# Performance work log

Measured on AMD Instinct MI355X. Metric: run time of the kernel, lower is better.

## Reference

```python
import jax, jax.numpy as jnp
import numpy as np
from jax import lax

TOPN = 4
CAT_NUM = 4
NUM_CLS = 200
PAD = 224
IMG = 448
HP = IMG + 2 * PAD  # 896
CROP = 224
IOU_THRESH = 0.25


def _gen_edge_anchors():
    # generate_default_anchor_maps: 3 pyramid levels; anchors ordered (anchor, h, w)
    # per level to match the channel-first flatten of ProposalNet tidy outputs.
    settings = [
        (32, 48.0, [2 ** (1. / 3.), 2 ** (2. / 3.)], [0.667, 1.0, 1.5]),
        (64, 96.0, [2 ** (1. / 3.), 2 ** (2. / 3.)], [0.667, 1.0, 1.5]),
        (128, 192.0, [1.0, 2 ** (1. / 3.), 2 ** (2. / 3.)], [0.667, 1.0, 1.5]),
    ]
    blocks = []
    for stride, size, scales, ars in settings:
        n = int(np.ceil(IMG / stride))
        c = np.arange(n, dtype=np.float64) * stride + stride / 2.0
        cy, cx = np.meshgrid(c, c, indexing='ij')
        for sc in scales:
            for ar in ars:
                h = size * sc / np.sqrt(ar)
                w = size * sc * np.sqrt(ar)
                a = np.stack([cy - h / 2., cx - w / 2., cy + h / 2., cx + w / 2.], axis=-1)
                blocks.append(a.reshape(-1, 4))
    e = np.concatenate(blocks, axis=0)  # [1614, 4] (y0,x0,y1,x1)
    return (e + PAD).astype(np.int32)   # offset into padded image, truncated to int


EDGE_ANCHORS = _gen_edge_anchors()


def _conv(x, w, b, stride, pad):
    y = lax.conv_general_dilated(x, w, (stride, stride), [(pad, pad), (pad, pad)],
                                 dimension_numbers=('NCHW', 'OIHW', 'NCHW'))
    return y + b[None, :, None, None]


def _proposal_net(x, d1w, d1b, d2w, d2b, d3w, d3b, t1w, t1b, t2w, t2b, t3w, t3b):
    B = x.shape[0]
    d1 = jax.nn.relu(_conv(x, d1w, d1b, 1, 1))   # [B,128,14,14]
    d2 = jax.nn.relu(_conv(d1, d2w, d2b, 2, 1))  # [B,128,7,7]
    d3 = jax.nn.relu(_conv(d2, d3w, d3b, 2, 1))  # [B,128,4,4]
    t1 = _conv(d1, t1w, t1b, 1, 0).reshape(B, -1)  # 6*14*14 = 1176
    t2 = _conv(d2, t2w, t2b, 1, 0).reshape(B, -1)  # 6*7*7  = 294
    t3 = _conv(d3, t3w, t3b, 1, 0).reshape(B, -1)  # 9*4*4  = 144
    return jnp.concatenate([t1, t2, t3], axis=1)   # [B,1614]


def _hard_nms(scores, boxes, area):
    # Greedy hard NMS over A anchors, returns TOPN kept indices (score-desc order).
    A = scores.shape[0]

    def body(k, carry):
        mask, idxs = carry
        i = jnp.argmax(jnp.where(mask, scores, -jnp.inf))
        b = boxes[i]
        yy0 = jnp.maximum(boxes[:, 0], b[0])
        xx0 = jnp.maximum(boxes[:, 1], b[1])
        yy1 = jnp.minimum(boxes[:, 2], b[2])
        xx1 = jnp.minimum(boxes[:, 3], b[3])
        inter = jnp.maximum(yy1 - yy0, 0.) * jnp.maximum(xx1 - xx0, 0.)
        iou = inter / (area + area[i] - inter)
        mask = (mask & (iou < IOU_THRESH)).at[i].set(False)
        return mask, idxs.at[k].set(i.astype(jnp.int32))

    _, idxs = lax.fori_loop(0, TOPN, body, (jnp.ones((A,), bool), jnp.zeros((TOPN,), jnp.int32)))
    return idxs


def _crop_resize(img, box):
    # img [3,HP,HP], box [4] float (integer-valued). Bilinear, align_corners=True:
    # src coord = y0 + i*(h-1)/(CROP-1) over the slice [y0:y1).
    y0, x0, y1, x1 = box[0], box[1], box[2], box[3]
    t = jnp.arange(CROP, dtype=jnp.float32) / (CROP - 1.)
    ys = y0 + t * (y1 - y0 - 1.)
    xs = x0 + t * (x1 - x0 - 1.)
    yi0 = jnp.clip(jnp.floor(ys).astype(jnp.int32), 0, HP - 1)
    xi0 = jnp.clip(jnp.floor(xs).astype(jnp.int32), 0, HP - 1)
    yi1 = jnp.minimum(yi0 + 1, HP - 1)
    xi1 = jnp.minimum(xi0 + 1, HP - 1)
    wy = (ys - yi0.astype(jnp.float32))[None, :, None]
    wx = (xs - xi0.astype(jnp.float32))[None, None, :]
    r0 = img[:, yi0, :]
    r1 = img[:, yi1, :]
    rows = r0 + (r1 - r0) * wy          # [3,CROP,HP]
    c0 = rows[:, :, xi0]
    c1 = rows[:, :, xi1]
    return c0 + (c1 - c0) * wx          # [3,CROP,CROP]


def reference(x, rpn_feature, feature, resnet_out,
              down1_w, down1_b, down2_w, down2_b, down3_w, down3_b,
              tidy1_w, tidy1_b, tidy2_w, tidy2_b, tidy3_w, tidy3_b,
              feat_w, feat_b, partcls_w, partcls_b, concat_w, concat_b):
    B = x.shape[0]
    boxes_f = jnp.asarray(EDGE_ANCHORS, jnp.float32)
    area = (boxes_f[:, 2] - boxes_f[:, 0]) * (boxes_f[:, 3] - boxes_f[:, 1])

    rpn_score = _proposal_net(lax.stop_gradient(rpn_feature),
                              down1_w, down1_b, down2_w, down2_b, down3_w, down3_b,
                              tidy1_w, tidy1_b, tidy2_w, tidy2_b, tidy3_w, tidy3_b)
    scores_sg = lax.stop_gradient(rpn_score)
    top_idx = jax.vmap(lambda s: _hard_nms(s, boxes_f, area))(scores_sg)   # [B,TOPN]
    top_n_prob = jnp.take_along_axis(rpn_score, top_idx, axis=1)           # [B,TOPN]

    x_pad = jnp.pad(x, ((0, 0), (0, 0), (PAD, PAD), (PAD, PAD)))           # [B,3,896,896]
    sel_boxes = boxes_f[top_idx]                                           # [B,TOPN,4]
    part_imgs = jax.vmap(lambda img, bxs: jax.vmap(lambda b: _crop_resize(img, b))(bxs))(x_pad, sel_boxes)
    part_imgs = lax.stop_gradient(part_imgs).reshape(B * TOPN, 3, CROP, CROP)  # detach()

    # per-crop feature trunk (stand-in for shared ResNet50): strided 7x7 conv + GAP
    pf = jax.nn.relu(_conv(part_imgs, feat_w, feat_b, 32, 3)).mean(axis=(2, 3))  # [B*TOPN,2048]
    part_logits = (pf @ partcls_w.T + partcls_b).reshape(B, TOPN, NUM_CLS)
    part_feature = pf.reshape(B, TOPN, -1)[:, :CAT_NUM].reshape(B, -1)           # [B,4*2048]
    concat_out = jnp.concatenate([part_feature, feature], axis=1)                # [B,10240]
    concat_logits = concat_out @ concat_w.T + concat_b
    return resnet_out, concat_logits, part_logits, top_idx, top_n_prob


def setup_inputs():
    key = jax.random.key(0)
    ks = jax.random.split(key, 13)
    B = 16
    n = lambda k, shp, s=1.0: jax.random.normal(k, shp, jnp.float32) * s
    z = lambda c: jnp.zeros((c,), jnp.float32)
    return {
        'x': n(ks[0], (B, 3, 448, 448)),
        'rpn_feature': jax.nn.relu(n(ks[1], (B, 2048, 14, 14))),
        'feature': n(ks[2], (B, 2048)),
        'resnet_out': n(ks[3], (B, 200)),
        'down1_w': n(ks[4], (128, 2048, 3, 3), 0.01),
        'down1_b': z(128),
        'down2_w': n(ks[5], (128, 128, 3, 3), 0.03),
        'down2_b': z(128),
        'down3_w': n(ks[6], (128, 128, 3, 3), 0.03),
        'down3_b': z(128),
        'tidy1_w': n(ks[7], (6, 128, 1, 1), 0.1),
        'tidy1_b': z(6),
        'tidy2_w': n(ks[8], (6, 128, 1, 1), 0.1),
        'tidy2_b': z(6),
        'tidy3_w': n(ks[9], (9, 128, 1, 1), 0.1),
        'tidy3_b': z(9),
        'feat_w': n(ks[10], (2048, 3, 7, 7), 0.05),
        'feat_b': z(2048),
        'partcls_w': n(ks[11], (200, 2048), 0.02),
        'partcls_b': z(200),
        'concat_w': n(ks[12], (200, 2048 * (CAT_NUM + 1)), 0.01),
        'concat_b': z(200),
    }
```

## Files before the change

### kernel.cpp

```cpp
#include <hip/hip_runtime.h>
#include <math.h>

#define NANCH 1614
#define A1 1176
#define A2 1470
#define KSPLIT 4
#define N_D1E (16*128*196)

#define OFF_D1 0
#define OFF_D2 401408
#define OFF_D3 501760
#define OFF_SC 534528
#define OFF_PF 560352
#define OFF_P  691424
#define OFF_INT 1152416
#define OFF_BIG 1158944
#define SZ_AT 3211264
#define SZ_BW 1179648
#define OFF_ATH (OFF_BIG)
#define OFF_ATL (OFF_ATH + SZ_AT)
#define OFF_BWH (OFF_ATL + SZ_AT)
#define OFF_BWL (OFF_BWH + SZ_BW)
#define OFF_PM  (OFF_BWL + SZ_BW)
#define SZ_PM   3612672
#define TOTAL_MFMA_F (OFF_PM + SZ_PM)
#define N_D2E (16*128*49)
#define N_D3E (16*128*16)
#define OFF_P2 OFF_BIG
#define OFF_P3 (OFF_BIG + 4*N_D2E)

#define OUT_CONCAT 3200
#define OUT_PART   6400
#define OUT_TIDX   19200
#define OUT_TPROB  19264

typedef __attribute__((ext_vector_type(8))) short short8;
typedef __attribute__((ext_vector_type(4))) float f32x4;

__device__ __forceinline__ unsigned short bf16_rn(float f) {
    unsigned u = __float_as_uint(f);
    unsigned r = u + 0x7fffu + ((u >> 16) & 1u);
    return (unsigned short)(r >> 16);
}
__device__ __forceinline__ float bf16_to_f(unsigned short h) {
    return __uint_as_float(((unsigned)h) << 16);
}

__global__ void anchor_kernel(int* __restrict__ anc) {
    int i = blockIdx.x * 256 + threadIdx.x;
    if (i >= NANCH) return;
    int stride, n, sgroup, j;
    double size;
    if (i < A1)      { stride = 32;  size = 48.0;  n = 14; j = i;      sgroup = 0; }
    else if (i < A2) { stride = 64;  size = 96.0;  n = 7;  j = i - A1; sgroup = 0; }
    else             { stride = 128; size = 192.0; n = 4;  j = i - A2; sgroup = 1; }
    int cells = n * n;
    int combo = j / cells, cell = j % cells;
    int sc_i = combo / 3, ar_i = combo % 3;
    double sc;
    if (sgroup == 0) sc = pow(2.0, (double)(sc_i + 1) / 3.0);
    else             sc = (sc_i == 0) ? 1.0 : pow(2.0, (double)sc_i / 3.0);
    double ar = (ar_i == 0) ? 0.667 : ((ar_i == 1) ? 1.0 : 1.5);
    int y = cell / n, x = cell % n;
    double cy = (double)y * stride + stride / 2.0;
    double cx = (double)x * stride + stride / 2.0;
    double sq = sqrt(ar);
    double h = size * sc / sq, w = size * sc * sq;
    anc[i*4+0] = (int)(cy - h/2.0 + 224.0);
    anc[i*4+1] = (int)(cx - w/2.0 + 224.0);
    anc[i*4+2] = (int)(cy + h/2.0 + 224.0);
    anc[i*4+3] = (int)(cx + w/2.0 + 224.0);
}

__launch_bounds__(256)
__global__ void split_rpn_t(const float* __restrict__ rpn,
                            unsigned short* __restrict__ ath, unsigned short* __restrict__ atl) {
    __shared__ float T[32*197];
    int b = blockIdx.x >> 6, icb = blockIdx.x & 63;
    int tid = threadIdx.x;
    for (int idx = tid; idx < 32*196; idx += 256) {
        int i = idx / 196, s = idx % 196;
        T[i*197 + s] = rpn[((size_t)(b*2048 + icb*32 + i))*196 + s];
    }
    __syncthreads();
    for (int idx = tid; idx < 32*196; idx += 256) {
        int s = idx >> 5, i = idx & 31;
        float f = T[i*197 + s];
        unsigned short hi = bf16_rn(f);
        unsigned short lo = bf16_rn(f - bf16_to_f(hi));
        size_t o = ((size_t)(b*196 + s))*2048 + icb*32 + i;
        ath[o] = hi; atl[o] = lo;
    }
}

__global__ void split_w(const float* __restrict__ w1,
                        unsigned short* __restrict__ bwh, unsigned short* __restrict__ bwl) {
    int idx = blockIdx.x * 256 + threadIdx.x;
    if (idx >= 9*128*2048) return;
    int tap = idx / (128*2048);
    int rem = idx % (128*2048);
    int oc = rem >> 11, ic = rem & 2047;
    float f = w1[((size_t)(oc*2048 + ic))*9 + tap];
    unsigned short hi = bf16_rn(f);
    unsigned short lo = bf16_rn(f - bf16_to_f(hi));
    bwh[idx] = hi; bwl[idx] = lo;
}

__launch_bounds__(256)
__global__ void d1_mfma(const unsigned short* __restrict__ ath, const unsigned short* __restrict__ atl,
                        const unsigned short* __restrict__ bwh, const unsigned short* __restrict__ bwl,
                        float* __restrict__ partM) {
    __shared__ unsigned short Ah[32*40], Al[32*40], Bh[128*40], Bl[128*40];
    int tid = threadIdx.x;
    int mb = blockIdx.x % 98, tap = blockIdx.x / 98;
    int dy = tap/3 - 1, dx = tap%3 - 1;
    int wave = tid >> 6, lane = tid & 63;
    int wr = wave >> 1, wc = wave & 1;
    int lg = lane >> 4, lr = lane & 15;

    int ar = tid >> 3, ahalf = (tid >> 2) & 1, aslot = tid & 3;
    int grow = mb*32 + ar;
    int b = grow / 196, s = grow % 196;
    int y = s / 14, x = s % 14;
    int ys = y + dy, xs = x + dx;
    bool avalid = (ys >= 0) && (ys < 14) && (xs >= 0) && (xs < 14);
    const unsigned short* asrc = (ahalf ? atl : ath)
        + ((size_t)(b*196 + (avalid ? (ys*14 + xs) : 0)))*2048 + aslot*8;
    unsigned short* adst = (ahalf ? Al : Ah) + ar*40 + aslot*8;

    const unsigned short* bsrc[4]; unsigned short* bdst[4];
#pragma unroll
    for (int rep = 0; rep < 4; ++rep) {
        int idx = rep*256 + tid;
        int half = idx >> 9, u = idx & 511, oc = u >> 2, slot = u & 3;
        bsrc[rep] = (half ? bwl : bwh) + ((size_t)(tap*128 + oc))*2048 + slot*8;
        bdst[rep] = (half ? Bl : Bh) + oc*40 + slot*8;
    }

    f32x4 acc[4];
#pragma unroll
    for (int f = 0; f < 4; ++f) acc[f] = (f32x4){0.f, 0.f, 0.f, 0.f};
    const short8 zer = {0,0,0,0,0,0,0,0};

    short8 ga, gb[4];
    ga = avalid ? *(const short8*)(asrc) : zer;
#pragma unroll
    for (int rep = 0; rep < 4; ++rep) gb[rep] = *(const short8*)(bsrc[rep]);

    for (int step = 0; step < 64; ++step) {
        __syncthreads();
        *(short8*)adst = ga;
#pragma unroll
        for (int rep = 0; rep < 4; ++rep) *(short8*)bdst[rep] = gb[rep];
        __syncthreads();
        if (step + 1 < 64) {
            int ic0 = (step + 1) * 32;
            ga = avalid ? *(const short8*)(asrc + ic0) : zer;
#pragma unroll
            for (int rep = 0; rep < 4; ++rep) gb[rep] = *(const short8*)(bsrc[rep] + ic0);
        }
        short8 a_h = *(const short8*)&Ah[(wr*16 + lr)*40 + lg*8];
        short8 a_l = *(const short8*)&Al[(wr*16 + lr)*40 + lg*8];
#pragma unroll
        for (int f = 0; f < 4; ++f) {
            int oc = wc*64 + f*16 + lr;
            short8 b_h = *(const short8*)&Bh[oc*40 + lg*8];
            short8 b_l = *(const short8*)&Bl[oc*40 + lg*8];
            acc[f] = __builtin_amdgcn_mfma_f32_16x16x32_bf16(a_h, b_h, acc[f], 0, 0, 0);
            acc[f] = __builtin_amdgcn_mfma_f32_16x16x32_bf16(a_h, b_l, acc[f], 0, 0, 0);
            acc[f] = __builtin_amdgcn_mfma_f32_16x16x32_bf16(a_l, b_h, acc[f], 0, 0, 0);
        }
    }
#pragma unroll
    for (int f = 0; f < 4; ++f) {
        int oc = wc*64 + f*16 + lr;
#pragma unroll
        for (int r = 0; r < 4; ++r) {
            int row = mb*32 + wr*16 + lg*4 + r;
            partM[((size_t)tap*3136 + row)*128 + oc] = acc[f][r];
        }
    }
}

__global__ void d1_combine(const float* __restrict__ partM, const float* __restrict__ b1,
                           float* __restrict__ d1) {
    int idx = blockIdx.x*256 + threadIdx.x;
    if (idx >= 3136*128) return;
    int oc = idx & 127, row = idx >> 7;
    float s = 0.f;
#pragma unroll
    for (int t = 0; t < 9; ++t) s += partM[(size_t)t*3136*128 + idx];
    int b = row / 196, sp = row % 196;
    d1[(b*128 + oc)*196 + sp] = fmaxf(s + b1[oc], 0.f);
}

__launch_bounds__(256)
__global__ void conv_d1_part(const float* __restrict__ rpn, const float* __restrict__ w1,
                             float* __restrict__ part) {
    __shared__ float lin[8*256];
    __shared__ float lwT[576];
    int tid = threadIdx.x;
    int ks = blockIdx.x & 3;
    int tile = (blockIdx.x >> 2) & 15;
    int b = blockIdx.x >> 6;
    int py = tid >> 4, px = tid & 15;
    bool pvalid = (py >= 1) && (py <= 14) && (px >= 1) && (px <= 14);
    int in_off = (b*2048)*196 + (py-1)*14 + (px-1);
    const float* wb = w1 + tile*8*18432;
    int s = tid, y = s / 14, x = s % 14;
    bool active = s < 196;
    float acc[8];
#pragma unroll
    for (int o = 0; o < 8; ++o) acc[o] = 0.f;
    float pv[8]; float wv[3];
    int c0 = ks * 64;
#pragma unroll
    for (int i = 0; i < 8; ++i) pv[i] = pvalid ? rpn[in_off + (c0*8 + i)*196] : 0.f;
#pragma unroll
    for (int r = 0; r < 3; ++r) {
        int u = tid + r*256;
        if (u < 576) { int oc = u/72, rem = u%72; wv[r] = wb[oc*18432 + c0*72 + rem]; }
    }
    for (int c = 0; c < 64; ++c) {
#pragma unroll
        for (int i = 0; i < 8; ++i) lin[i*256 + tid] = pv[i];
#pragma unroll
        for (int r = 0; r < 3; ++r) {
            int u = tid + r*256;
            if (u < 576) { int oc = u/72, rem = u%72; lwT[rem*8 + oc] = wv[r]; }
        }
        __syncthreads();
        if (c + 1 < 64) {
            int icb = (c0 + c + 1) * 8;
#pragma unroll
            for (int i = 0; i < 8; ++i) pv[i] = pvalid ? rpn[in_off + (icb + i)*196] : 0.f;
#pragma unroll
            for (int r = 0; r < 3; ++r) {
                int u = tid + r*256;
                if (u < 576) { int oc = u/72, rem = u%72; wv[r] = wb[oc*18432 + icb*9 + rem]; }
            }
        }
        if (active) {
#pragma unroll
            for (int ic = 0; ic < 8; ++ic) {
                int base = ic*256 + y*16 + x;
                float p[9];
                p[0]=lin[base+0];  p[1]=lin[base+1];  p[2]=lin[base+2];
                p[3]=lin[base+16]; p[4]=lin[base+17]; p[5]=lin[base+18];
                p[6]=lin[base+32]; p[7]=lin[base+33]; p[8]=lin[base+34];
#pragma unroll
                for (int k = 0; k < 9; ++k) {
                    const float4 wa  = *(const float4*)&lwT[(ic*9 + k)*8];
                    const float4 wb4 = *(const float4*)&lwT[(ic*9 + k)*8 + 4];
                    acc[0] += p[k]*wa.x;  acc[1] += p[k]*wa.y;
                    acc[2] += p[k]*wa.z;  acc[3] += p[k]*wa.w;
                    acc[4] += p[k]*wb4.x; acc[5] += p[k]*wb4.y;
                    acc[6] += p[k]*wb4.z; acc[7] += p[k]*wb4.w;
                }
            }
        }
        __syncthreads();
    }
    if (active) {
#pragma unroll
        for (int o = 0; o < 8; ++o) {
            int oc = tile*8 + o;
            part[ks*N_D1E + (b*128 + oc)*196 + s] = acc[o];
        }
    }
}

__global__ void d1_reduce(const float* __restrict__ part, const float* __restrict__ b1,
                          float* __restrict__ d1) {
    int idx = blockIdx.x * 256 + threadIdx.x;
    if (idx >= N_D1E) return;
    int oc = (idx / 196) & 127;
    float s = part[idx] + part[idx + N_D1E] + part[idx + 2*N_D1E] + part[idx + 3*N_D1E];
    d1[idx] = fmaxf(s + b1[oc], 0.f);
}

__launch_bounds__(256)
__global__ void conv_d2_part(const float* __restrict__ d1, const float* __restrict__ w2,
                             float* __restrict__ part) {
    __shared__ float lin[8*320];
    __shared__ float lwT[72*32];
    int tid = threadIdx.x;
    int ks = blockIdx.x & 3;
    int octile = (blockIdx.x >> 2) & 3;
    int b = blockIdx.x >> 4;
    int py = tid >> 4, px = tid & 15;
    bool pvalid = (py >= 1) && (py <= 14) && (px >= 1) && (px <= 14);
    int in_base = (b*128)*196 + (py-1)*14 + (px-1);
    int g = tid >> 6, s = tid & 63;
    int yo = s / 7, xo = s % 7;
    bool active = s < 49;
    const float* wb = w2 + (octile*32)*1152 + ks*288;

    float acc[8];
#pragma unroll
    for (int o = 0; o < 8; ++o) acc[o] = 0.f;
    float pv[8], wv[9];
#pragma unroll
    for (int i = 0; i < 8; ++i) pv[i] = pvalid ? d1[in_base + (ks*32 + i)*196] : 0.f;
#pragma unroll
    for (int r = 0; r < 9; ++r) {
        int u = tid + r*256; int oc_l = u/72, rem = u%72;
        wv[r] = wb[oc_l*1152 + rem];
    }
    for (int c = 0; c < 4; ++c) {
#pragma unroll
        for (int i = 0; i < 8; ++i) lin[i*320 + py*20 + px] = pv[i];
#pragma unroll
        for (int r = 0; r < 9; ++r) {
            int u = tid + r*256; int oc_l = u/72, rem = u%72;
            lwT[rem*32 + oc_l] = wv[r];
        }
        __syncthreads();
        if (c + 1 < 4) {
            int ic0 = ks*32 + (c+1)*8;
#pragma unroll
            for (int i = 0; i < 8; ++i) pv[i] = pvalid ? d1[in_base + (ic0 + i)*196] : 0.f;
#pragma unroll
            for (int r = 0; r < 9; ++r) {
                int u = tid + r*256; int oc_l = u/72, rem = u%72;
                wv[r] = wb[oc_l*1152 + (c+1)*72 + rem];
            }
        }
        if (active) {
#pragma unroll
            for (int ic = 0; ic < 8; ++ic) {
                int base = ic*320 + (2*yo)*20 + 2*xo;
                float p[9];
                p[0]=lin[base+0];  p[1]=lin[base+1];  p[2]=lin[base+2];
                p[3]=lin[base+20]; p[4]=lin[base+21]; p[5]=lin[base+22];
                p[6]=lin[base+40]; p[7]=lin[base+41]; p[8]=lin[base+42];
#pragma unroll
                for (int k = 0; k < 9; ++k) {
                    const float4 wa  = *(const float4*)&lwT[(ic*9 + k)*32 + g*8];
                    const float4 wb4 = *(const float4*)&lwT[(ic*9 + k)*32 + g*8 + 4];
                    acc[0] += p[k]*wa.x;  acc[1] += p[k]*wa.y;
                    acc[2] += p[k]*wa.z;  acc[3] += p[k]*wa.w;
                    acc[4] += p[k]*wb4.x; acc[5] += p[k]*wb4.y;
                    acc[6] += p[k]*wb4.z; acc[7] += p[k]*wb4.w;
                }
            }
        }
        __syncthreads();
    }
    if (active) {
#pragma unroll
        for (int o = 0; o < 8; ++o) {
            int oc = octile*32 + g*8 + o;
            part[ks*N_D2E + (b*128 + oc)*49 + s] = acc[o];
        }
    }
}

__launch_bounds__(256)
__global__ void conv_d3_part(const float* __restrict__ d2, const float* __restrict__ w3,
                             float* __restrict__ part) {
    __shared__ float lin3[8*108];
    __shared__ float lwT3[72*128];
    int tid = threadIdx.x;
    int ks = blockIdx.x & 15;
    int b = blockIdx.x >> 4;
    int g = tid >> 4, s = tid & 15;
    int yo = s >> 2, xo = s & 3;

    for (int r = 0; r < 4; ++r) {
        int u = tid + r*256;
        if (u < 864) {
            int ic = u / 108, rem = u % 108;
            int ty = rem / 12, tx = rem % 12;
            int iy = ty - 1, ix = tx - 1;
            float v = 0.f;
            if (iy >= 0 && iy < 7 && ix >= 0 && ix < 7)
                v = d2[(b*128 + ks*8 + ic)*49 + iy*7 + ix];
            lin3[u] = v;
        }
    }
#pragma unroll
    for (int r = 0; r < 36; ++r) {
        int u = tid + r*256;
        int oc_l = u / 72, rem = u % 72;
        lwT3[rem*128 + oc_l] = w3[oc_l*1152 + ks*72 + rem];
    }
    __syncthreads();

    float acc[8];
#pragma unroll
    for (int o = 0; o < 8; ++o) acc[o] = 0.f;
#pragma unroll
    for (int ic = 0; ic < 8; ++ic) {
        int base = ic*108 + (2*yo)*12 + 2*xo;
        float p[9];
        p[0]=lin3[base+0];  p[1]=lin3[base+1];  p[2]=lin3[base+2];
        p[3]=lin3[base+12]; p[4]=lin3[base+13]; p[5]=lin3[base+14];
        p[6]=lin3[base+24]; p[7]=lin3[base+25]; p[8]=lin3[base+26];
#pragma unroll
        for (int k = 0; k < 9; ++k) {
            const float4 wa  = *(const float4*)&lwT3[(ic*9 + k)*128 + g*8];
            const float4 wb4 = *(const float4*)&lwT3[(ic*9 + k)*128 + g*8 + 4];
            acc[0] += p[k]*wa.x;  acc[1] += p[k]*wa.y;
            acc[2] += p[k]*wa.z;  acc[3] += p[k]*wa.w;
            acc[4] += p[k]*wb4.x; acc[5] += p[k]*wb4.y;
            acc[6] += p[k]*wb4.z; acc[7] += p[k]*wb4.w;
        }
    }
#pragma unroll
    for (int o = 0; o < 8; ++o) {
        int oc = g*8 + o;
        part[ks*N_D3E + (b*128 + oc)*16 + s] = acc[o];
    }
}

__global__ void reduce_relu(const float* __restrict__ part, const float* __restrict__ bias,
                            float* __restrict__ out, int nsplit, int N, int SP) {
    int idx = blockIdx.x*256 + threadIdx.x;
    if (idx >= N) return;
    int oc = (idx / SP) & 127;
    float s = 0.f;
    for (int p = 0; p < nsplit; ++p) s += part[p*N + idx];
    out[idx] = fmaxf(s + bias[oc], 0.f);
}

__global__ void tidy_kernel(const float* __restrict__ d1, const float* __restrict__ d2, const float* __restrict__ d3,
                            const float* __restrict__ t1w, const float* __restrict__ t1b,
                            const float* __restrict__ t2w, const float* __restrict__ t2b,
                            const float* __restrict__ t3w, const float* __restrict__ t3b,
                            float* __restrict__ scores) {
    int idx = blockIdx.x * 256 + threadIdx.x;
    if (idx >= 16*NANCH) return;
    int b = idx / NANCH, i = idx % NANCH;
    const float* src; const float* tw; const float* tb; int S, c, s;
    if (i < A1)      { c = i/196;           s = i%196;        src = d1 + b*128*196 + s; S = 196; tw = t1w; tb = t1b; }
    else if (i < A2) { int j = i - A1; c = j/49; s = j%49;    src = d2 + b*128*49  + s; S = 49;  tw = t2w; tb = t2b; }
    else             { int j = i - A2; c = j/16; s = j%16;    src = d3 + b*128*16  + s; S = 16;  tw = t3w; tb = t3b; }
    float acc = tb[c];
    const float* wr = tw + c*128;
    for (int ic = 0; ic < 128; ++ic) acc += src[ic*S] * wr[ic];
    scores[idx] = acc;
}

__launch_bounds__(256)
__global__ void nms_kernel(const float* __restrict__ scores, const int* __restrict__ anc,
                           int* __restrict__ topidx, float* __restrict__ out) {
    __shared__ float s[NANCH];
    __shared__ float by0[NANCH], bx0[NANCH], by1[NANCH], bx1[NANCH], ar[NANCH];
    __shared__ float rv[256]; __shared__ int ri[256];
    __shared__ int sel[4];
    int b = blockIdx.x, tid = threadIdx.x;
    for (int j = tid; j < NANCH; j += 256) {
        s[j] = scores[b*NANCH + j];
        float y0 = (float)anc[j*4+0], x0 = (float)anc[j*4+1];
        float y1 = (float)anc[j*4+2], x1 = (float)anc[j*4+3];
        by0[j] = y0; bx0[j] = x0; by1[j] = y1; bx1[j] = x1;
        ar[j] = (y1 - y0) * (x1 - x0);
    }
    __syncthreads();
    for (int k = 0; k < 4; ++k) {
        float bv = -INFINITY; int bi = NANCH;
        for (int j = tid; j < NANCH; j += 256) {
            float v = s[j];
            if (v > bv) { bv = v; bi = j; }
        }
        rv[tid] = bv; ri[tid] = bi;
        __syncthreads();
        for (int off = 128; off > 0; off >>= 1) {
            if (tid < off) {
                float v2 = rv[tid+off]; int i2 = ri[tid+off];
                if (v2 > rv[tid] || (v2 == rv[tid] && i2 < ri[tid])) { rv[tid] = v2; ri[tid] = i2; }
            }
            __syncthreads();
        }
        int i = ri[0];
        if (tid == 0) sel[k] = i;
        float a0 = by0[i], a1 = bx0[i], a2 = by1[i], a3 = bx1[i], ai = ar[i];
        for (int j = tid; j < NANCH; j += 256) {
            float yy0 = fmaxf(by0[j], a0), xx0 = fmaxf(bx0[j], a1);
            float yy1 = fminf(by1[j], a2), xx1 = fminf(bx1[j], a3);
            float inter = fmaxf(yy1 - yy0, 0.f) * fmaxf(xx1 - xx0, 0.f);
            float iou = inter / (ar[j] + ai - inter);
            if (!(iou < 0.25f)) s[j] = -INFINITY;
        }
        if (tid == 0) s[i] = -INFINITY;
        __syncthreads();
    }
    if (tid < 4) {
        int i = sel[tid];
        topidx[b*4 + tid] = i;
        out[OUT_TIDX  + b*4 + tid] = (float)i;
        out[OUT_TPROB + b*4 + tid] = scores[b*NANCH + i];
    }
}

__device__ __forceinline__ float fetchpix(const float* img, int Y, int X) {
    if (Y >= 224 && Y < 672 && X >= 224 && X < 672) return img[(Y - 224)*448 + (X - 224)];
    return 0.f;
}

__global__ void sampler_kernel(const float* __restrict__ x, const int* __restrict__ anc,
                               const int* __restrict__ topidx, float* __restrict__ P) {
    int crop = blockIdx.x >> 2;
    int b = crop >> 2;
    int idx = topidx[crop];
    float y0 = (float)anc[idx*4+0], x0 = (float)anc[idx*4+1];
    float y1 = (float)anc[idx*4+2], x1 = (float)anc[idx*4+3];
    float dy = y1 - y0 - 1.0f, dx = x1 - x0 - 1.0f;
    const float* imgb = x + b*3*448*448;
    for (int u = (blockIdx.x & 3)*256 + threadIdx.x; u < 7203; u += 1024) {
        int c = u / 2401; int rem = u % 2401;
        int rid = rem / 49, cid = rem % 49;
        int oy = rid/7, ky = rid%7, ox = cid/7, kx = cid%7;
        int rr = 32*oy - 3 + ky, cc = 32*ox - 3 + kx;
        float val = 0.f;
        if (rr >= 0 && cc >= 0) {
            float ty = (float)rr / 223.0f;
            float ys = __fadd_rn(y0, __fmul_rn(ty, dy));
            int yi0 = (int)floorf(ys); yi0 = yi0 < 0 ? 0 : (yi0 > 895 ? 895 : yi0);
            int yi1 = (yi0 + 1 > 895) ? 895 : yi0 + 1;
            float wy = ys - (float)yi0;
            float tx = (float)cc / 223.0f;
            float xs = __fadd_rn(x0, __fmul_rn(tx, dx));
            int xi0 = (int)floorf(xs); xi0 = xi0 < 0 ? 0 : (xi0 > 895 ? 895 : xi0);
            int xi1 = (xi0 + 1 > 895) ? 895 : xi0 + 1;
            float wx = xs - (float)xi0;
            const float* img = imgb + c*448*448;
            float p00 = fetchpix(img, yi0, xi0), p10 = fetchpix(img, yi1, xi0);
            float p01 = fetchpix(img, yi0, xi1), p11 = fetchpix(img, yi1, xi1);
            float r0 = p00 + (p10 - p00)*wy;
            float r1 = p01 + (p11 - p01)*wy;
            val = r0 + (r1 - r0)*wx;
        }
        int pos = oy*7 + ox, kk = c*49 + ky*7 + kx;
        P[crop*7203 + pos*147 + kk] = val;
    }
}

__launch_bounds__(256)
__global__ void feat_gemm_kernel(const float* __restrict__ P, const float* __restrict__ fw,
                                 const float* __restrict__ fb, float* __restrict__ pf) {
    __shared__ float lp[49*148];
    int crop = blockIdx.x >> 3, tile = blockIdx.x & 7;
    int oc = tile*256 + threadIdx.x;
    for (int u = threadIdx.x; u < 7203; u += 256)
        lp[(u/147)*148 + (u%147)] = P[crop*7203 + u];
    __syncthreads();
    float s[49];
#pragma unroll
    for (int p = 0; p < 49; ++p) s[p] = 0.f;
    const float* wr = fw + oc*147;
    for (int kc = 0; kc < 36; ++kc) {
        float w0 = wr[kc*4], w1 = wr[kc*4+1], w2 = wr[kc*4+2], w3 = wr[kc*4+3];
#pragma unroll
        for (int p = 0; p < 49; ++p) {
            float4 v = *(const float4*)&lp[p*148 + kc*4];
            s[p] += v.x*w0 + v.y*w1 + v.z*w2 + v.w*w3;
        }
    }
    {
        float w0 = wr[144], w1 = wr[145], w2 = wr[146];
#pragma unroll
        for (int p = 0; p < 49; ++p)
            s[p] += lp[p*148+144]*w0 + lp[p*148+145]*w1 + lp[p*148+146]*w2;
    }
    float bias = fb[oc], acc = 0.f;
#pragma unroll
    for (int p = 0; p < 49; ++p) acc += fmaxf(s[p] + bias, 0.f);
    pf[crop*2048 + oc] = acc / 49.0f;
}

__global__ void partcls_kernel(const float* __restrict__ pf, const float* __restrict__ pw,
                               const float* __restrict__ pb, float* __restrict__ out) {
    int o = blockIdx.x; int crop = o / 200, cls = o % 200;
    int lane = threadIdx.x;
    const float* a = pf + crop*2048; const float* w = pw + cls*2048;
    float sum = 0.f;
#pragma unroll
    for (int i = 0; i < 8; ++i) {
        int k = lane*4 + i*256;
        float4 a4 = *(const float4*)&a[k];
        float4 w4 = *(const float4*)&w[k];
        sum += a4.x*w4.x + a4.y*w4.y + a4.z*w4.z + a4.w*w4.w;
    }
#pragma unroll
    for (int off = 32; off > 0; off >>= 1) sum += __shfl_down(sum, off);
    if (lane == 0) out[OUT_PART + o] = sum + pb[cls];
}

__launch_bounds__(256)
__global__ void concat_kernel(const float* __restrict__ pf, const float* __restrict__ feature,
                              const float* __restrict__ cw, const float* __restrict__ cb,
                              float* __restrict__ out) {
    __shared__ float red[4][16];
    int j = blockIdx.x, tid = threadIdx.x;
    const float* w = cw + (size_t)j*10240;
    float acc[16];
#pragma unroll
    for (int b = 0; b < 16; ++b) acc[b] = 0.f;
    for (int k = tid; k < 10240; k += 256) {
        float wk = w[k];
        const float* v; int stride;
        if (k < 8192) { v = pf + k; stride = 8192; }
        else          { v = feature + (k - 8192); stride = 2048; }
#pragma unroll
        for (int b = 0; b < 16; ++b) acc[b] += v[b*stride] * wk;
    }
#pragma unroll
    for (int b = 0; b < 16; ++b) {
        float s2 = acc[b];
#pragma unroll
        for (int off = 32; off > 0; off >>= 1) s2 += __shfl_down(s2, off);
        if ((tid & 63) == 0) red[tid >> 6][b] = s2;
    }
    __syncthreads();
    if (tid < 16)
        out[OUT_CONCAT + tid*200 + j] = red[0][tid] + red[1][tid] + red[2][tid] + red[3][tid] + cb[j];
}

extern "C" void kernel_launch(void* const* d_in, const int* in_sizes, int n_in,
                              void* d_out, int out_size, void* d_ws, size_t ws_size,
                              hipStream_t stream) {
    const float* x    = (const float*)d_in[0];
    const float* rpn  = (const float*)d_in[1];
    const float* feat = (const float*)d_in[2];
    const float* rout = (const float*)d_in[3];
    const float* d1w  = (const float*)d_in[4];
    const float* d1b  = (const float*)d_in[5];
    const float* d2w  = (const float*)d_in[6];
    const float* d2b  = (const float*)d_in[7];
    const float* d3w  = (const float*)d_in[8];
    const float* d3b  = (const float*)d_in[9];
    const float* t1w  = (const float*)d_in[10];
    const float* t1b  = (const float*)d_in[11];
    const float* t2w  = (const float*)d_in[12];
    const float* t2b  = (const float*)d_in[13];
    const float* t3w  = (const float*)d_in[14];
    const float* t3b  = (const float*)d_in[15];
    const float* fw   = (const float*)d_in[16];
    const float* fbb  = (const float*)d_in[17];
    const float* pw   = (const float*)d_in[18];
    const float* pb   = (const float*)d_in[19];
    const float* cw   = (const float*)d_in[20];
    const float* cb   = (const float*)d_in[21];
    float* out = (float*)d_out;
    float* wsf = (float*)d_ws;
    float* d1  = wsf + OFF_D1;
    float* d2  = wsf + OFF_D2;
    float* d3  = wsf + OFF_D3;
    float* sc  = wsf + OFF_SC;
    float* pfb = wsf + OFF_PF;
    float* P   = wsf + OFF_P;
    int* anc    = (int*)(wsf + OFF_INT);
    int* topidx = anc + NANCH*4;

    hipMemcpyAsync(out, rout, 3200*sizeof(float), hipMemcpyDeviceToDevice, stream);

    anchor_kernel<<<7, 256, 0, stream>>>(anc);

    bool use_mfma = ws_size >= (size_t)TOTAL_MFMA_F * sizeof(float);
    if (use_mfma) {
        unsigned short* ath = (unsigned short*)(wsf + OFF_ATH);
        unsigned short* atl = (unsigned short*)(wsf + OFF_ATL);
        unsigned short* bwh = (unsigned short*)(wsf + OFF_BWH);
        unsigned short* bwl = (unsigned short*)(wsf + OFF_BWL);
        float* pm = wsf + OFF_PM;
        split_rpn_t<<<1024, 256, 0, stream>>>(rpn, ath, atl);
        split_w<<<9216, 256, 0, stream>>>(d1w, bwh, bwl);
        d1_mfma<<<98*9, 256, 0, stream>>>(ath, atl, bwh, bwl, pm);
        d1_combine<<<(3136*128 + 255)/256, 256, 0, stream>>>(pm, d1b, d1);
    } else {
        float* part = wsf + OFF_BIG;
        conv_d1_part<<<16*16*KSPLIT, 256, 0, stream>>>(rpn, d1w, part);
        d1_reduce<<<(N_D1E + 255)/256, 256, 0, stream>>>(part, d1b, d1);
    }

    float* part2 = wsf + OFF_P2;
    float* part3 = wsf + OFF_P3;
    conv_d2_part<<<256, 256, 0, stream>>>(d1, d2w, part2);
    reduce_relu<<<(N_D2E + 255)/256, 256, 0, stream>>>(part2, d2b, d2, 4, N_D2E, 49);
    conv_d3_part<<<256, 256, 0, stream>>>(d2, d3w, part3);
    reduce_relu<<<(N_D3E + 255)/256, 256, 0, stream>>>(part3, d3b, d3, 16, N_D3E, 16);

    tidy_kernel<<<101, 256, 0, stream>>>(d1, d2, d3, t1w, t1b, t2w, t2b, t3w, t3b, sc);
    nms_kernel<<<16, 256, 0, stream>>>(sc, anc, topidx, out);
    sampler_kernel<<<256, 256, 0, stream>>>(x, anc, topidx, P);
    feat_gemm_kernel<<<512, 256, 0, stream>>>(P, fw, fbb, pfb);
    partcls_kernel<<<12800, 64, 0, stream>>>(pfb, pw, pb, out);
    concat_kernel<<<200, 256, 0, stream>>>(pfb, feat, cw, cb, out);
}
```

Baseline: 412.4 us.

## Double-buffer LDS and widen M tile to 64 rows in d1 MFMA conv

The d1 MFMA kernel now gives each block 64 output rows instead of 32, so every wave computes two 16-row fragments that share the same B-weight fragments. This halves how often the weight tile is reloaded per output and halves the grid to 441 blocks. Shared memory is double-buffered so the next K-step's global loads are written to the alternate buffer while MFMAs run, needing one barrier per step instead of two. The cost is more LDS and accumulator registers, which may lower occupancy, and fewer blocks for the CUs to share.

```diff
diff --git a/kernel.cpp b/kernel.cpp
--- a/kernel.cpp
+++ b/kernel.cpp
@@ -106,78 +106,109 @@
     bwh[idx] = hi; bwl[idx] = lo;
 }
 
+#define ABUF (64*40)
+#define BBUF (128*40)
 __launch_bounds__(256)
 __global__ void d1_mfma(const unsigned short* __restrict__ ath, const unsigned short* __restrict__ atl,
                         const unsigned short* __restrict__ bwh, const unsigned short* __restrict__ bwl,
                         float* __restrict__ partM) {
-    __shared__ unsigned short Ah[32*40], Al[32*40], Bh[128*40], Bl[128*40];
+    __shared__ unsigned short Ah[2*ABUF], Al[2*ABUF], Bh[2*BBUF], Bl[2*BBUF];
     int tid = threadIdx.x;
-    int mb = blockIdx.x % 98, tap = blockIdx.x / 98;
+    int tap = blockIdx.x / 49, mb = blockIdx.x % 49;
     int dy = tap/3 - 1, dx = tap%3 - 1;
     int wave = tid >> 6, lane = tid & 63;
     int wr = wave >> 1, wc = wave & 1;
     int lg = lane >> 4, lr = lane & 15;
 
-    int ar = tid >> 3, ahalf = (tid >> 2) & 1, aslot = tid & 3;
-    int grow = mb*32 + ar;
-    int b = grow / 196, s = grow % 196;
-    int y = s / 14, x = s % 14;
-    int ys = y + dy, xs = x + dx;
-    bool avalid = (ys >= 0) && (ys < 14) && (xs >= 0) && (xs < 14);
-    const unsigned short* asrc = (ahalf ? atl : ath)
-        + ((size_t)(b*196 + (avalid ? (ys*14 + xs) : 0)))*2048 + aslot*8;
-    unsigned short* adst = (ahalf ? Al : Ah) + ar*40 + aslot*8;
-
+    const unsigned short* asrc[2]; unsigned short* adst[2]; bool avalid[2];
+#pragma unroll
+    for (int rep = 0; rep < 2; ++rep) {
+        int idx = rep*256 + tid;
+        int rw = idx >> 3, half = (idx >> 2) & 1, slot = idx & 3;
+        int grow = mb*64 + rw;
+        int b = grow / 196, s = grow % 196;
+        int y = s / 14, x = s % 14;
+        int ys = y + dy, xs = x + dx;
+        bool av = (ys >= 0) && (ys < 14) && (xs >= 0) && (xs < 14);
+        avalid[rep] = av;
+        asrc[rep] = (half ? atl : ath)
+            + ((size_t)(b*196 + (av ? (ys*14 + xs) : 0)))*2048 + slot*8;
+        adst[rep] = (half ? Al : Ah) + rw*40 + slot*8;
+    }
     const unsigned short* bsrc[4]; unsigned short* bdst[4];
 #pragma unroll
     for (int rep = 0; rep < 4; ++rep) {
         int idx = rep*256 + tid;
-        int half = idx >> 9, u = idx & 511, oc = u >> 2, slot = u & 3;
+        int oc = idx >> 3, half = (idx >> 2) & 1, slot = idx & 3;
         bsrc[rep] = (half ? bwl : bwh) + ((size_t)(tap*128 + oc))*2048 + slot*8;
         bdst[rep] = (half ? Bl : Bh) + oc*40 + slot*8;
     }
 
-    f32x4 acc[4];
-#pragma unroll
-    for (int f = 0; f < 4; ++f) acc[f] = (f32x4){0.f, 0.f, 0.f, 0.f};
+    f32x4 acc[2][4];
+#pragma unroll
+    for (int r2 = 0; r2 < 2; ++r2)
+#pragma unroll
+        for (int f = 0; f < 4; ++f) acc[r2][f] = (f32x4){0.f, 0.f, 0.f, 0.f};
     const short8 zer = {0,0,0,0,0,0,0,0};
 
-    short8 ga, gb[4];
-    ga = avalid ? *(const short8*)(asrc) : zer;
+    short8 ga[2], gb[4];
+#pragma unroll
+    for (int rep = 0; rep < 2; ++rep) ga[rep] = avalid[rep] ? *(const short8*)(asrc[rep]) : zer;
 #pragma unroll
     for (int rep = 0; rep < 4; ++rep) gb[rep] = *(const short8*)(bsrc[rep]);
+#pragma unroll
+    for (int rep = 0; rep < 2; ++rep) *(short8*)(adst[rep]) = ga[rep];
+#pragma unroll
+    for (int rep = 0; rep < 4; ++rep) *(short8*)(bdst[rep]) = gb[rep];
+    __syncthreads();
+
+    int abase_w = wr*32*40 + lr*40 + lg*8;
+    int bbase_w = wc*64*40 + lg*8;
 
     for (int step = 0; step < 64; ++step) {
-        __syncthreads();
-        *(short8*)adst = ga;
-#pragma unroll
-        for (int rep = 0; rep < 4; ++rep) *(short8*)bdst[rep] = gb[rep];
-        __syncthreads();
+        int buf = step & 1;
         if (step + 1 < 64) {
             int ic0 = (step + 1) * 32;
-            ga = avalid ? *(const short8*)(asrc + ic0) : zer;
+#pragma unroll
+            for (int rep = 0; rep < 2; ++rep) ga[rep] = avalid[rep] ? *(const short8*)(asrc[rep] + ic0) : zer;
 #pragma unroll
             for (int rep = 0; rep < 4; ++rep) gb[rep] = *(const short8*)(bsrc[rep] + ic0);
         }
-        short8 a_h = *(const short8*)&Ah[(wr*16 + lr)*40 + lg*8];
-        short8 a_l = *(const short8*)&Al[(wr*16 + lr)*40 + lg*8];
+        int ab = buf*ABUF, bb = buf*BBUF;
+        short8 ah0 = *(const short8*)&Ah[ab + abase_w];
+        short8 ah1 = *(const short8*)&Ah[ab + abase_w + 16*40];
+        short8 al0 = *(const short8*)&Al[ab + abase_w];
+        short8 al1 = *(const short8*)&Al[ab + abase_w + 16*40];
 #pragma unroll
         for (int f = 0; f < 4; ++f) {
-            int oc = wc*64 + f*16 + lr;
-            short8 b_h = *(const short8*)&Bh[oc*40 + lg*8];
-            short8 b_l = *(const short8*)&Bl[oc*40 + lg*8];
-            acc[f] = __builtin_amdgcn_mfma_f32_16x16x32_bf16(a_h, b_h, acc[f], 0, 0, 0);
-            acc[f] = __builtin_amdgcn_mfma_f32_16x16x32_bf16(a_h, b_l, acc[f], 0, 0, 0);
-            acc[f] = __builtin_amdgcn_mfma_f32_16x16x32_bf16(a_l, b_h, acc[f], 0, 0, 0);
-        }
-    }
+            int bo = bb + bbase_w + (f*16 + lr)*40;
+            short8 b_h = *(const short8*)&Bh[bo];
+            short8 b_l = *(const short8*)&Bl[bo];
+            acc[0][f] = __builtin_amdgcn_mfma_f32_16x16x32_bf16(ah0, b_h, acc[0][f], 0, 0, 0);
+            acc[0][f] = __builtin_amdgcn_mfma_f32_16x16x32_bf16(ah0, b_l, acc[0][f], 0, 0, 0);
+            acc[0][f] = __builtin_amdgcn_mfma_f32_16x16x32_bf16(al0, b_h, acc[0][f], 0, 0, 0);
+            acc[1][f] = __builtin_amdgcn_mfma_f32_16x16x32_bf16(ah1, b_h, acc[1][f], 0, 0, 0);
+            acc[1][f] = __builtin_amdgcn_mfma_f32_16x16x32_bf16(ah1, b_l, acc[1][f], 0, 0, 0);
+            acc[1][f] = __builtin_amdgcn_mfma_f32_16x16x32_bf16(al1, b_h, acc[1][f], 0, 0, 0);
+        }
+        if (step + 1 < 64) {
+            int nb = buf ^ 1;
+#pragma unroll
+            for (int rep = 0; rep < 2; ++rep) *(short8*)(adst[rep] + nb*ABUF) = ga[rep];
+#pragma unroll
+            for (int rep = 0; rep < 4; ++rep) *(short8*)(bdst[rep] + nb*BBUF) = gb[rep];
+        }
+        __syncthreads();
+    }
+#pragma unroll
+    for (int r2 = 0; r2 < 2; ++r2)
 #pragma unroll
     for (int f = 0; f < 4; ++f) {
         int oc = wc*64 + f*16 + lr;
 #pragma unroll
         for (int r = 0; r < 4; ++r) {
-            int row = mb*32 + wr*16 + lg*4 + r;
-            partM[((size_t)tap*3136 + row)*128 + oc] = acc[f][r];
+            int row = mb*64 + wr*32 + r2*16 + lg*4 + r;
+            partM[((size_t)tap*3136 + row)*128 + oc] = acc[r2][f][r];
         }
     }
 }
@@ -667,7 +698,7 @@
         float* pm = wsf + OFF_PM;
         split_rpn_t<<<1024, 256, 0, stream>>>(rpn, ath, atl);
         split_w<<<9216, 256, 0, stream>>>(d1w, bwh, bwl);
-        d1_mfma<<<98*9, 256, 0, stream>>>(ath, atl, bwh, bwl, pm);
+        d1_mfma<<<441, 256, 0, stream>>>(ath, atl, bwh, bwl, pm);
         d1_combine<<<(3136*128 + 255)/256, 256, 0, stream>>>(pm, d1b, d1);
     } else {
         float* part = wsf + OFF_BIG;
```

Result: faster. 391.4 us (-5.1%).
